# Performance work log

Measured on AMD Instinct MI355X. Metric: run time of the kernel, lower is better.

## Reference

```python
import jax, jax.numpy as jnp
import numpy as np

Q = 128          # number of slices
S = 1024 // Q    # slice length = 8
U = 32           # hidden units per slice
EPS = 1e-3       # keras LayerNormalization default epsilon


def setup_inputs() -> dict:
    key = jax.random.key(0)
    ks = jax.random.split(key, 8)
    B = 16384
    x = jax.random.normal(ks[0], (B, 1, 1, Q * S), dtype=jnp.float32)
    # per-slice Dense1 (S->U), LayerNorm(gamma,beta), Dense2 (U->1)
    W1 = jax.random.normal(ks[1], (Q, S, U), dtype=jnp.float32) / np.sqrt(S)
    b1 = jnp.zeros((Q, U), dtype=jnp.float32)
    gamma = jnp.ones((Q, U), dtype=jnp.float32)
    beta = jnp.zeros((Q, U), dtype=jnp.float32)
    W2 = jax.random.normal(ks[2], (Q, U), dtype=jnp.float32) / np.sqrt(U)
    b2 = jnp.zeros((Q,), dtype=jnp.float32)
    return {"x": x, "W1": W1, "b1": b1, "gamma": gamma, "beta": beta,
            "W2": W2, "b2": b2}


def reference(x, W1, b1, gamma, beta, W2, b2):
    B = x.shape[0]
    xs = x.reshape(B, Q, S)                              # (B,Q,S)
    # batched tiny Dense -> ELU
    h = jnp.einsum('bqs,qsu->bqu', xs, W1) + b1          # (B,Q,U)
    h = jax.nn.elu(h)
    # per-slice LayerNorm over last axis
    mu = jnp.mean(h, axis=-1, keepdims=True)
    var = jnp.mean(jnp.square(h - mu), axis=-1, keepdims=True)
    h = (h - mu) * jax.lax.rsqrt(var + EPS) * gamma + beta
    # batched output projection U -> 1, concat over slices
    out = jnp.einsum('bqu,qu->bq', h, W2) + b2           # (B,Q)
    return out
```

## Files before the change

kernel.cpp:

```cpp
#include <hip/hip_runtime.h>


typedef __attribute__((ext_vector_type(8))) short short8;
typedef __attribute__((ext_vector_type(16))) float f32x16;

__device__ __forceinline__ short fbits(__bf16 b) { return __builtin_bit_cast(short, b); }

__device__ __forceinline__ float elu1(float v) {
    return v > 0.f ? v : __expf(v) - 1.f;
}

__device__ __forceinline__ short8 cvt8(const float4& a, const float4& b) {
    short8 r;
    r[0] = fbits((__bf16)a.x); r[1] = fbits((__bf16)a.y);
    r[2] = fbits((__bf16)a.z); r[3] = fbits((__bf16)a.w);
    r[4] = fbits((__bf16)b.x); r[5] = fbits((__bf16)b.y);
    r[6] = fbits((__bf16)b.z); r[7] = fbits((__bf16)b.w);
    return r;
}

__device__ __forceinline__ float finish(const f32x16& acc, const f32x16& g2r,
                                        float G, float C) {
    float sum = 0.f, ss = 0.f, dot = 0.f;
    #pragma unroll
    for (int r = 0; r < 16; ++r) {
        float e = elu1(acc[r]);
        sum += e;
        ss  = fmaf(e, e, ss);
        dot = fmaf(e, g2r[r], dot);
    }
    sum += __shfl_xor(sum, 32);
    ss  += __shfl_xor(ss, 32);
    dot += __shfl_xor(dot, 32);
    float mu  = sum * 0.03125f;
    float var = fmaf(-mu, mu, ss * 0.03125f);
    float inv = rsqrtf(var + 1e-3f);
    return fmaf(inv, fmaf(-mu, G, dot), C);
}

__global__ __launch_bounds__(256, 4) void divenc_mfma(
    const float* __restrict__ x,
    const float* __restrict__ W1,
    const float* __restrict__ b1,
    const float* __restrict__ gamma,
    const float* __restrict__ beta,
    const float* __restrict__ W2,
    const float* __restrict__ b2,
    float* __restrict__ out)
{
    __shared__ float lout[512 * 5];

    const int tid  = threadIdx.x;
    const int w    = tid >> 6;
    const int ln   = tid & 63;
    const int u    = ln & 31;
    const int half = ln >> 5;
    const int qt   = blockIdx.y;
    const int q    = qt * 4 + w;
    const int bx   = blockIdx.x;

    short8 wfrag;
    #pragma unroll
    for (int j = 0; j < 8; ++j) {
        float f  = W1[q * 256 + j * 32 + u];
        __bf16 h = (__bf16)f;
        wfrag[j] = half ? fbits((__bf16)(f - (float)h)) : fbits(h);
    }

    f32x16 biasr, g2r;
    float G, C;
    {
        float gs = 0.f, cs = 0.f;
        #pragma unroll
        for (int c = 0; c < 4; ++c) {
            const int ub = q * 32 + 4 * half + 8 * c;
            float4 b1v = *(const float4*)&b1[ub];
            float4 gav = *(const float4*)&gamma[ub];
            float4 w2v = *(const float4*)&W2[ub];
            float4 bev = *(const float4*)&beta[ub];
            #pragma unroll
            for (int j = 0; j < 4; ++j) {
                float g2 = ((const float*)&gav)[j] * ((const float*)&w2v)[j];
                biasr[4 * c + j] = ((const float*)&b1v)[j];
                g2r[4 * c + j]   = g2;
                gs += g2;
                cs += ((const float*)&bev)[j] * ((const float*)&w2v)[j];
            }
        }
        gs += __shfl_xor(gs, 32);
        cs += __shfl_xor(cs, 32);
        G = gs;
        C = cs + b2[q];
    }

    const float* xq = x + q * 8;

    float4 c00, c01, c10, c11;
    {
        const float* p0 = xq + (size_t)(bx * 512 + u) * 1024;
        const float* p1 = xq + (size_t)(bx * 512 + 32 + u) * 1024;
        c00 = ((const float4*)p0)[0]; c01 = ((const float4*)p0)[1];
        c10 = ((const float4*)p1)[0]; c11 = ((const float4*)p1)[1];
    }

    #pragma unroll 1
    for (int it = 0; it < 8; ++it) {
        const int b0 = it * 64;

        const int bn = (it < 7) ? b0 + 64 : b0;
        const float* pn0 = xq + (size_t)(bx * 512 + bn + u) * 1024;
        const float* pn1 = xq + (size_t)(bx * 512 + bn + 32 + u) * 1024;
        float4 n00 = ((const float4*)pn0)[0], n01 = ((const float4*)pn0)[1];
        float4 n10 = ((const float4*)pn1)[0], n11 = ((const float4*)pn1)[1];

        short8 xa = cvt8(c00, c01);
        short8 xb = cvt8(c10, c11);

        f32x16 acc0 = __builtin_amdgcn_mfma_f32_32x32x16_bf16(wfrag, xa, biasr, 0, 0, 0);
        f32x16 acc1 = __builtin_amdgcn_mfma_f32_32x32x16_bf16(wfrag, xb, biasr, 0, 0, 0);

        float res0 = finish(acc0, g2r, G, C);
        float res1 = finish(acc1, g2r, G, C);

        if (half == 0) {
            lout[(b0 + u) * 5 + w]      = res0;
            lout[(b0 + 32 + u) * 5 + w] = res1;
        }

        c00 = n00; c01 = n01; c10 = n10; c11 = n11;
    }

    __syncthreads();

    {
        const int r0 = tid;
        const int r1 = tid + 256;
        float4 o0, o1;
        o0.x = lout[r0 * 5 + 0]; o0.y = lout[r0 * 5 + 1];
        o0.z = lout[r0 * 5 + 2]; o0.w = lout[r0 * 5 + 3];
        o1.x = lout[r1 * 5 + 0]; o1.y = lout[r1 * 5 + 1];
        o1.z = lout[r1 * 5 + 2]; o1.w = lout[r1 * 5 + 3];
        *(float4*)(out + (size_t)(bx * 512 + r0) * 128 + qt * 4) = o0;
        *(float4*)(out + (size_t)(bx * 512 + r1) * 128 + qt * 4) = o1;
    }
}

extern "C" void kernel_launch(void* const* d_in, const int* in_sizes, int n_in,
                              void* d_out, int out_size, void* d_ws, size_t ws_size,
                              hipStream_t stream) {
    const float* x     = (const float*)d_in[0];
    const float* W1    = (const float*)d_in[1];
    const float* b1    = (const float*)d_in[2];
    const float* gamma = (const float*)d_in[3];
    const float* beta  = (const float*)d_in[4];
    const float* W2    = (const float*)d_in[5];
    const float* b2    = (const float*)d_in[6];
    float* out = (float*)d_out;

    dim3 grid(32, 32);
    divenc_mfma<<<grid, 256, 0, stream>>>(x, W1, b1, gamma, beta, W2, b2, out);
}
```

Before: 32.21 us.

## Stage x panels through double-buffered LDS as bf16 and halve rows per block

Each block now loads a contiguous 128-byte panel of x per row, covering the four slices it handles, with coalesced float4 loads. It converts the panel to bf16 once and stores it in a padded, double-buffered LDS tile that all four waves read their MFMA operands from. Each block now covers 256 rows instead of 512, so the grid doubles and more blocks are in flight. In exchange it adds a __syncthreads per iteration and extra LDS traffic.

```diff
diff --git a/kernel.cpp b/kernel.cpp
--- a/kernel.cpp
+++ b/kernel.cpp
@@ -3,6 +3,8 @@
 
 typedef __attribute__((ext_vector_type(8))) short short8;
 typedef __attribute__((ext_vector_type(16))) float f32x16;
+
+#define XS_STRIDE 40
 
 __device__ __forceinline__ short fbits(__bf16 b) { return __builtin_bit_cast(short, b); }
 
@@ -10,12 +12,10 @@
     return v > 0.f ? v : __expf(v) - 1.f;
 }
 
-__device__ __forceinline__ short8 cvt8(const float4& a, const float4& b) {
-    short8 r;
-    r[0] = fbits((__bf16)a.x); r[1] = fbits((__bf16)a.y);
-    r[2] = fbits((__bf16)a.z); r[3] = fbits((__bf16)a.w);
-    r[4] = fbits((__bf16)b.x); r[5] = fbits((__bf16)b.y);
-    r[6] = fbits((__bf16)b.z); r[7] = fbits((__bf16)b.w);
+__device__ __forceinline__ short4 cvt4(float4 v) {
+    short4 r;
+    r.x = fbits((__bf16)v.x); r.y = fbits((__bf16)v.y);
+    r.z = fbits((__bf16)v.z); r.w = fbits((__bf16)v.w);
     return r;
 }
 
@@ -48,7 +48,8 @@
     const float* __restrict__ b2,
     float* __restrict__ out)
 {
-    __shared__ float lout[512 * 5];
+    __shared__ short xs[2][64 * XS_STRIDE];
+    __shared__ float lout[256 * 5];
 
     const int tid  = threadIdx.x;
     const int w    = tid >> 6;
@@ -58,6 +59,12 @@
     const int qt   = blockIdx.y;
     const int q    = qt * 4 + w;
     const int bx   = blockIdx.x;
+    const int band = bx * 256;
+
+    const int srow0 = tid >> 3;
+    const int srow1 = srow0 + 32;
+    const int schk  = tid & 7;
+    const float* xpan = x + qt * 32 + schk * 4;
 
     short8 wfrag;
     #pragma unroll
@@ -93,28 +100,27 @@
         C = cs + b2[q];
     }
 
-    const float* xq = x + q * 8;
-
-    float4 c00, c01, c10, c11;
     {
-        const float* p0 = xq + (size_t)(bx * 512 + u) * 1024;
-        const float* p1 = xq + (size_t)(bx * 512 + 32 + u) * 1024;
-        c00 = ((const float4*)p0)[0]; c01 = ((const float4*)p0)[1];
-        c10 = ((const float4*)p1)[0]; c11 = ((const float4*)p1)[1];
+        float4 g0 = *(const float4*)(xpan + (size_t)(band + srow0) * 1024);
+        float4 g1 = *(const float4*)(xpan + (size_t)(band + srow1) * 1024);
+        *(short4*)&xs[0][srow0 * XS_STRIDE + schk * 4] = cvt4(g0);
+        *(short4*)&xs[0][srow1 * XS_STRIDE + schk * 4] = cvt4(g1);
     }
+    __syncthreads();
 
     #pragma unroll 1
-    for (int it = 0; it < 8; ++it) {
-        const int b0 = it * 64;
+    for (int it = 0; it < 4; ++it) {
+        const int cur = it & 1;
+        const int b0  = it * 64;
 
-        const int bn = (it < 7) ? b0 + 64 : b0;
-        const float* pn0 = xq + (size_t)(bx * 512 + bn + u) * 1024;
-        const float* pn1 = xq + (size_t)(bx * 512 + bn + 32 + u) * 1024;
-        float4 n00 = ((const float4*)pn0)[0], n01 = ((const float4*)pn0)[1];
-        float4 n10 = ((const float4*)pn1)[0], n11 = ((const float4*)pn1)[1];
+        float4 g0, g1;
+        if (it < 3) {
+            g0 = *(const float4*)(xpan + (size_t)(band + b0 + 64 + srow0) * 1024);
+            g1 = *(const float4*)(xpan + (size_t)(band + b0 + 64 + srow1) * 1024);
+        }
 
-        short8 xa = cvt8(c00, c01);
-        short8 xb = cvt8(c10, c11);
+        short8 xa = *(const short8*)&xs[cur][u * XS_STRIDE + w * 8];
+        short8 xb = *(const short8*)&xs[cur][(u + 32) * XS_STRIDE + w * 8];
 
         f32x16 acc0 = __builtin_amdgcn_mfma_f32_32x32x16_bf16(wfrag, xa, biasr, 0, 0, 0);
         f32x16 acc1 = __builtin_amdgcn_mfma_f32_32x32x16_bf16(wfrag, xb, biasr, 0, 0, 0);
@@ -127,21 +133,20 @@
             lout[(b0 + 32 + u) * 5 + w] = res1;
         }
 
-        c00 = n00; c01 = n01; c10 = n10; c11 = n11;
+        if (it < 3) {
+            *(short4*)&xs[cur ^ 1][srow0 * XS_STRIDE + schk * 4] = cvt4(g0);
+            *(short4*)&xs[cur ^ 1][srow1 * XS_STRIDE + schk * 4] = cvt4(g1);
+        }
+        __syncthreads();
     }
 
-    __syncthreads();
-
     {
-        const int r0 = tid;
-        const int r1 = tid + 256;
-        float4 o0, o1;
-        o0.x = lout[r0 * 5 + 0]; o0.y = lout[r0 * 5 + 1];
-        o0.z = lout[r0 * 5 + 2]; o0.w = lout[r0 * 5 + 3];
-        o1.x = lout[r1 * 5 + 0]; o1.y = lout[r1 * 5 + 1];
-        o1.z = lout[r1 * 5 + 2]; o1.w = lout[r1 * 5 + 3];
-        *(float4*)(out + (size_t)(bx * 512 + r0) * 128 + qt * 4) = o0;
-        *(float4*)(out + (size_t)(bx * 512 + r1) * 128 + qt * 4) = o1;
+        float4 o;
+        o.x = lout[tid * 5 + 0];
+        o.y = lout[tid * 5 + 1];
+        o.z = lout[tid * 5 + 2];
+        o.w = lout[tid * 5 + 3];
+        *(float4*)(out + (size_t)(band + tid) * 128 + qt * 4) = o;
     }
 }
 
@@ -157,6 +162,6 @@
     const float* b2    = (const float*)d_in[6];
     float* out = (float*)d_out;
 
-    dim3 grid(32, 32);
+    dim3 grid(64, 32);
     divenc_mfma<<<grid, 256, 0, stream>>>(x, W1, b1, gamma, beta, W2, b2, out);
 }
```

After: 28.66 us. -11.0%, faster.
